# Optimization experiments

Measured on AMD Instinct MI355X. Metric: run time of the kernel, lower is better.

## Reference

```python
import jax, jax.numpy as jnp
import numpy as np

B, H, W, C = 16, 56, 56, 256
NH, WS, SS = 8, 7, 3          # heads, window size, shift size
HD = C // NH                  # head dim = 32
MLPD = 4 * C                  # mlp hidden = 1024
WA = WS * WS                  # window area = 49
NW = (H // WS) * (W // WS)    # windows per image = 64
SCALE = HD ** -0.5


def _rel_pos_index():
    coords = np.stack(np.meshgrid(np.arange(WS), np.arange(WS), indexing='ij'))
    cf = coords.reshape(2, -1)
    rel = (cf[:, :, None] - cf[:, None, :]).transpose(1, 2, 0)
    rel[:, :, 0] += WS - 1
    rel[:, :, 1] += WS - 1
    rel[:, :, 0] *= 2 * WS - 1
    return rel.sum(-1)  # (WA, WA) int


def _shift_attn_mask():
    img = np.zeros((H, W))
    cnt = 0
    for hs in (slice(0, -WS), slice(-WS, -SS), slice(-SS, None)):
        for ws_ in (slice(0, -WS), slice(-WS, -SS), slice(-SS, None)):
            img[hs, ws_] = cnt
            cnt += 1
    mw = img.reshape(H // WS, WS, W // WS, WS).transpose(0, 2, 1, 3).reshape(-1, WA)
    am = mw[:, None, :] - mw[:, :, None]
    return np.where(am != 0, -100.0, 0.0).astype(np.float32)  # (NW, WA, WA)

REL_IDX = jnp.asarray(_rel_pos_index())
ATTN_MASK = jnp.asarray(_shift_attn_mask())


def setup_inputs() -> dict:
    key = jax.random.key(0)
    ks = jax.random.split(key, 8)
    s = 0.02
    return {
        'x':      jax.random.normal(ks[0], (B, H * W, C), jnp.float32),
        'g1':     jnp.ones((C,), jnp.float32),
        'be1':    jnp.zeros((C,), jnp.float32),
        'w_qkv':  jax.random.normal(ks[1], (C, 3 * C), jnp.float32) * s,
        'b_qkv':  jnp.zeros((3 * C,), jnp.float32),
        'rpt':    jax.random.normal(ks[2], ((2 * WS - 1) ** 2, NH), jnp.float32) * s,
        'w_proj': jax.random.normal(ks[3], (C, C), jnp.float32) * s,
        'b_proj': jnp.zeros((C,), jnp.float32),
        'g2':     jnp.ones((C,), jnp.float32),
        'be2':    jnp.zeros((C,), jnp.float32),
        'w_fc1':  jax.random.normal(ks[4], (C, MLPD), jnp.float32) * s,
        'b_fc1':  jnp.zeros((MLPD,), jnp.float32),
        'w_fc2':  jax.random.normal(ks[5], (MLPD, C), jnp.float32) * s,
        'b_fc2':  jnp.zeros((C,), jnp.float32),
    }


def _ln(x, g, b, eps=1e-5):
    m = x.mean(-1, keepdims=True)
    v = ((x - m) ** 2).mean(-1, keepdims=True)
    return (x - m) * jax.lax.rsqrt(v + eps) * g + b


def reference(x, g1, be1, w_qkv, b_qkv, rpt, w_proj, b_proj, g2, be2,
              w_fc1, b_fc1, w_fc2, b_fc2):
    shortcut = x
    h = _ln(x, g1, be1).reshape(B, H, W, C)
    # cyclic shift
    h = jnp.roll(h, (-SS, -SS), axis=(1, 2))
    # window partition -> (B*NW, WA, C)
    h = h.reshape(B, H // WS, WS, W // WS, WS, C).transpose(0, 1, 3, 2, 4, 5)
    h = h.reshape(B * NW, WA, C)
    # qkv
    qkv = h @ w_qkv + b_qkv                       # (B*NW, WA, 3C)
    qkv = qkv.reshape(B * NW, WA, 3, NH, HD).transpose(2, 0, 3, 1, 4)
    q, k, v = qkv[0], qkv[1], qkv[2]              # (B*NW, NH, WA, HD)
    attn = jnp.einsum('wnqd,wnkd->wnqk', q * SCALE, k)   # (B*NW, NH, WA, WA)
    # relative position bias
    bias = rpt[REL_IDX.reshape(-1)].reshape(WA, WA, NH).transpose(2, 0, 1)
    attn = attn + bias[None]
    # shifted-window mask, per window
    attn = attn.reshape(B, NW, NH, WA, WA) + ATTN_MASK[None, :, None]
    attn = jax.nn.softmax(attn.reshape(B * NW, NH, WA, WA), axis=-1)
    out = jnp.einsum('wnqk,wnkd->wnqd', attn, v)  # (B*NW, NH, WA, HD)
    out = out.transpose(0, 2, 1, 3).reshape(B * NW, WA, C)
    out = out @ w_proj + b_proj
    # window reverse + unshift
    out = out.reshape(B, H // WS, W // WS, WS, WS, C).transpose(0, 1, 3, 2, 4, 5)
    out = out.reshape(B, H, W, C)
    out = jnp.roll(out, (SS, SS), axis=(1, 2)).reshape(B, H * W, C)
    x = shortcut + out
    # MLP block
    h2 = _ln(x, g2, be2)
    h2 = jax.nn.gelu(h2 @ w_fc1 + b_fc1, approximate=False) @ w_fc2 + b_fc2
    return x + h2
```

## Files before the change

### kernel.cpp

```cpp
#include <hip/hip_runtime.h>
#include <hip/hip_bf16.h>
#include <cstdint>
#include <cstddef>
#include <type_traits>

typedef __attribute__((ext_vector_type(8))) short short8;
typedef __attribute__((ext_vector_type(4))) float f32x4;
typedef __attribute__((ext_vector_type(4))) unsigned short us4;

#define DEVINL __device__ __forceinline__

static constexpr int SS_ = 3;
static constexpr int HH = 56, WW = 56;
#define SCALE_Q 0.17677669529663689f

DEVINL unsigned short f2b(float f) {
    unsigned int u = __builtin_bit_cast(unsigned int, f);
    unsigned int r = (u + 0x7FFFu + ((u >> 16) & 1u)) >> 16;
    return (unsigned short)r;
}
DEVINL float b2f(unsigned short s) {
    return __builtin_bit_cast(float, ((unsigned int)s) << 16);
}

DEVINL float gelu(float v) {
    float ax = fabsf(v) * 0.70710678118654752f;
    float t = 1.0f / (1.0f + 0.3275911f * ax);
    float poly = t * (0.254829592f +
                 t * (-0.284496736f +
                 t * (1.421413741f +
                 t * (-1.453152027f + t * 1.061405429f))));
    float e = __expf(-ax * ax);
    float erfv = 1.0f - poly * e;
    erfv = v >= 0.0f ? erfv : -erfv;
    return 0.5f * v * (1.0f + erfv);
}

DEVINL void gload_lds16(const unsigned short* g, unsigned short* l) {
    __builtin_amdgcn_global_load_lds(
        (const __attribute__((address_space(1))) unsigned int*)g,
        (__attribute__((address_space(3))) unsigned int*)l, 16, 0, 0);
}

__global__ void wconv_kernel(const float* __restrict__ in,
                             unsigned short* __restrict__ out, int K, int N) {
    int i = blockIdx.x * 256 + threadIdx.x;
    if (i >= K * N) return;
    int k = i / N, n = i - k * N;
    out[(size_t)n * K + k] = f2b(in[i]);
}

template <int MODE, typename TIN>
__global__ __launch_bounds__(256) void ln_kernel(
    const TIN* __restrict__ x, const float* __restrict__ g,
    const float* __restrict__ be, unsigned short* __restrict__ out) {
    const int wid = threadIdx.x >> 6, lane = threadIdx.x & 63;
    const int t = blockIdx.x * 4 + wid;
    int src;
    if constexpr (MODE == 1) {
        int w = t / 49, p = t - w * 49;
        int b = w >> 6, widx = w & 63;
        int wy = widx >> 3, wx = widx & 7;
        int py = p / 7, px = p - py * 7;
        int y = wy * 7 + py + SS_;  if (y >= HH) y -= HH;
        int xx = wx * 7 + px + SS_; if (xx >= WW) xx -= WW;
        src = b * (HH * WW) + y * WW + xx;
    } else {
        src = t;
    }
    float4 v;
    if constexpr (std::is_same_v<TIN, float>) {
        v = reinterpret_cast<const float4*>(x + (size_t)src * 256)[lane];
    } else {
        us4 u = reinterpret_cast<const us4*>(x + (size_t)src * 256)[lane];
        v.x = b2f(u.x); v.y = b2f(u.y); v.z = b2f(u.z); v.w = b2f(u.w);
    }
    float s = v.x + v.y + v.z + v.w;
    float q = v.x * v.x + v.y * v.y + v.z * v.z + v.w * v.w;
#pragma unroll
    for (int m = 1; m < 64; m <<= 1) {
        s += __shfl_xor(s, m);
        q += __shfl_xor(q, m);
    }
    float mean = s * (1.0f / 256.0f);
    float var = q * (1.0f / 256.0f) - mean * mean;
    float rs = rsqrtf(var + 1e-5f);
    int c = lane * 4;
    us4 o;
    o.x = f2b((v.x - mean) * rs * g[c + 0] + be[c + 0]);
    o.y = f2b((v.y - mean) * rs * g[c + 1] + be[c + 1]);
    o.z = f2b((v.z - mean) * rs * g[c + 2] + be[c + 2]);
    o.w = f2b((v.w - mean) * rs * g[c + 3] + be[c + 3]);
    *reinterpret_cast<us4*>(out + (size_t)t * 256 + c) = o;
}

template <int KDIM, int EPI>
__global__ __launch_bounds__(512) void gemm_kernel(
    const unsigned short* __restrict__ A, const unsigned short* __restrict__ Bt,
    const float* __restrict__ bias, void* __restrict__ out0,
    const void* __restrict__ res, unsigned short* __restrict__ o_q,
    unsigned short* __restrict__ o_k, unsigned short* __restrict__ o_v) {
    constexpr int BM = 256, BN = 128, BK = 32, NK = KDIM / BK;
    __shared__ __align__(16) unsigned short As[2][BM * BK];
    __shared__ __align__(16) unsigned short Bs[2][BN * BK];
    const int tid = threadIdx.x;
    const int wid = tid >> 6, lane = tid & 63;

    const int nwg = gridDim.x * gridDim.y;
    const int bid = blockIdx.x + gridDim.x * blockIdx.y;
    const int nb = (bid & 7) * (nwg >> 3) + (bid >> 3);
    const int n0 = (nb % gridDim.x) * BN;
    const int m0 = (nb / gridDim.x) * BM;

    const int wm = wid >> 1, wn = wid & 1;
    const int lr = lane & 15, kg = lane >> 4;
    f32x4 acc[4][4] = {};

    const int arow0 = tid >> 2, aslot = tid & 3;

    auto STAGE = [&](int kt, int buf) {
#pragma unroll
        for (int i = 0; i < 2; i++) {
            int row = i * 128 + arow0;
            int c = aslot ^ ((row >> 1) & 3);
            gload_lds16(A + (size_t)(m0 + row) * KDIM + kt * BK + c * 8,
                        As[buf] + i * 4096 + tid * 8);
        }
        {
            int row = arow0;
            int c = aslot ^ ((row >> 1) & 3);
            gload_lds16(Bt + (size_t)(n0 + row) * KDIM + kt * BK + c * 8,
                        Bs[buf] + tid * 8);
        }
    };

    STAGE(0, 0);
    __syncthreads();
    int cur = 0;
    for (int kt = 0; kt < NK; kt++) {
        if (kt + 1 < NK) STAGE(kt + 1, cur ^ 1);
        short8 a[4], b[4];
#pragma unroll
        for (int mf = 0; mf < 4; mf++) {
            int r = wm * 64 + mf * 16 + lr;
            a[mf] = *reinterpret_cast<const short8*>(
                As[cur] + r * 32 + ((kg ^ ((r >> 1) & 3)) << 3));
        }
#pragma unroll
        for (int nf = 0; nf < 4; nf++) {
            int r = wn * 64 + nf * 16 + lr;
            b[nf] = *reinterpret_cast<const short8*>(
                Bs[cur] + r * 32 + ((kg ^ ((r >> 1) & 3)) << 3));
        }
#pragma unroll
        for (int mf = 0; mf < 4; mf++)
#pragma unroll
            for (int nf = 0; nf < 4; nf++)
                acc[mf][nf] = __builtin_amdgcn_mfma_f32_16x16x32_bf16(
                    a[mf], b[nf], acc[mf][nf], 0, 0, 0);
        __syncthreads();
        cur ^= 1;
    }

#pragma unroll
    for (int mf = 0; mf < 4; mf++) {
#pragma unroll
        for (int nf = 0; nf < 4; nf++) {
#pragma unroll
            for (int j = 0; j < 4; j++) {
                int row = m0 + wm * 64 + mf * 16 + kg * 4 + j;
                int col = n0 + wn * 64 + nf * 16 + lr;
                float v = acc[mf][nf][j] + bias[col];
                if constexpr (EPI == 0) {
                    int w = row / 49, p = row - w * 49;
                    int which = col >> 8, h = (col >> 5) & 7, d = col & 31;
                    size_t th = (size_t)(w * 8 + h);
                    if (which == 0)
                        o_q[th * 1568 + p * 32 + d] = f2b(v * SCALE_Q);
                    else if (which == 1)
                        o_k[th * 1568 + p * 32 + d] = f2b(v);
                    else
                        o_v[th * 2048 + d * 64 + p] = f2b(v);
                } else if constexpr (EPI == 1) {
                    int w = row / 49, p = row - w * 49;
                    int b2 = w >> 6, widx = w & 63;
                    int wy = widx >> 3, wx = widx & 7;
                    int py = p / 7, px = p - py * 7;
                    int y = wy * 7 + py + SS_;  if (y >= HH) y -= HH;
                    int xx = wx * 7 + px + SS_; if (xx >= WW) xx -= WW;
                    size_t oi = ((size_t)(b2 * 3136 + y * 56 + xx)) * 256 + col;
                    reinterpret_cast<unsigned short*>(out0)[oi] =
                        f2b(v + reinterpret_cast<const float*>(res)[oi]);
                } else if constexpr (EPI == 2) {
                    reinterpret_cast<unsigned short*>(out0)[(size_t)row * 1024 + col] =
                        f2b(gelu(v));
                } else {
                    size_t oi = (size_t)row * 256 + col;
                    reinterpret_cast<float*>(out0)[oi] =
                        v + b2f(reinterpret_cast<const unsigned short*>(res)[oi]);
                }
            }
        }
    }
}

__global__ __launch_bounds__(256) void attn_kernel(
    const unsigned short* __restrict__ qg, const unsigned short* __restrict__ kgl,
    const unsigned short* __restrict__ vg, const float* __restrict__ rpt,
    unsigned short* __restrict__ out) {
    __shared__ __align__(16) unsigned short sm[4][6144];
    __shared__ unsigned short rpts[169 * 8];
    const int tid = threadIdx.x, wid = tid >> 6, lane = tid & 63;
    for (int i = tid; i < 169 * 8; i += 256) rpts[i] = f2b(rpt[i]);
    const int task = blockIdx.x * 4 + wid;
    const int w = task >> 3, h = task & 7;
    const int widx = w & 63, wy = widx >> 3, wx = widx & 7;
    unsigned short* q_s = sm[wid];
    unsigned short* k_s = sm[wid] + 2048;
    unsigned short* v_s = sm[wid] + 4096;
    unsigned short* p_s = sm[wid];
    const unsigned short* qsrc = qg + (size_t)task * 1568;
    const unsigned short* ksrc = kgl + (size_t)task * 1568;
    const unsigned short* vsrc = vg + (size_t)task * 2048;
    for (int c = lane; c < 196; c += 64) {
        int row = c >> 2, kc = c & 3;
        int off = (row * 32 + kc * 8) ^ ((row & 7) << 3);
        *reinterpret_cast<short8*>(q_s + off) =
            *reinterpret_cast<const short8*>(qsrc + c * 8);
        *reinterpret_cast<short8*>(k_s + off) =
            *reinterpret_cast<const short8*>(ksrc + c * 8);
    }
#pragma unroll
    for (int i = 0; i < 4; i++) {
        int c = i * 64 + lane;
        int row = c >> 3, kc = c & 7;
        int off = (row * 64 + kc * 8) ^ ((row & 7) << 3);
        *reinterpret_cast<short8*>(v_s + off) =
            *reinterpret_cast<const short8*>(vsrc + c * 8);
    }
    __syncthreads();

    const int lr = lane & 15, kg = lane >> 4;
    short8 af[4], bf[4];
#pragma unroll
    for (int mf = 0; mf < 4; mf++) {
        int r = mf * 16 + lr;
        af[mf] = *reinterpret_cast<const short8*>(
            q_s + ((r * 32 + kg * 8) ^ ((r & 7) << 3)));
    }
#pragma unroll
    for (int nf = 0; nf < 4; nf++) {
        int r = nf * 16 + lr;
        bf[nf] = *reinterpret_cast<const short8*>(
            k_s + ((r * 32 + kg * 8) ^ ((r & 7) << 3)));
    }
    f32x4 s[4][4] = {};
#pragma unroll
    for (int mf = 0; mf < 4; mf++)
#pragma unroll
        for (int nf = 0; nf < 4; nf++)
            s[mf][nf] = __builtin_amdgcn_mfma_f32_16x16x32_bf16(af[mf], bf[nf],
                                                                s[mf][nf], 0, 0, 0);
#pragma unroll
    for (int mf = 0; mf < 4; mf++) {
#pragma unroll
        for (int j = 0; j < 4; j++) {
            int row = mf * 16 + kg * 4 + j;
            bool rvalid = row < 49;
            int qy = 0, qx = 0, gq = 0;
            if (rvalid) {
                qy = row / 7; qx = row - qy * 7;
                int yi = wy * 7 + qy, xi = wx * 7 + qx;
                gq = ((yi < 49) ? 0 : ((yi < 53) ? 1 : 2)) * 3 +
                     ((xi < 49) ? 0 : ((xi < 53) ? 1 : 2));
            }
            float L[4];
#pragma unroll
            for (int nf = 0; nf < 4; nf++) {
                int col = nf * 16 + lr;
                float val = s[mf][nf][j];
                if (rvalid && col < 49) {
                    int ky = col / 7, kx = col - ky * 7;
                    int yi = wy * 7 + ky, xi = wx * 7 + kx;
                    int gk = ((yi < 49) ? 0 : ((yi < 53) ? 1 : 2)) * 3 +
                             ((xi < 49) ? 0 : ((xi < 53) ? 1 : 2));
                    val += b2f(rpts[((qy - ky + 6) * 13 + (qx - kx + 6)) * 8 + h]);
                    if (gq != gk) val -= 100.0f;
                } else {
                    val = -1e30f;
                }
                L[nf] = val;
            }
            float m = fmaxf(fmaxf(L[0], L[1]), fmaxf(L[2], L[3]));
#pragma unroll
            for (int t2 = 1; t2 < 16; t2 <<= 1) m = fmaxf(m, __shfl_xor(m, t2));
            float P[4], psum = 0.f;
#pragma unroll
            for (int nf = 0; nf < 4; nf++) {
                P[nf] = __expf(L[nf] - m);
                psum += P[nf];
            }
#pragma unroll
            for (int t2 = 1; t2 < 16; t2 <<= 1) psum += __shfl_xor(psum, t2);
            float inv = 1.0f / psum;
#pragma unroll
            for (int nf = 0; nf < 4; nf++) {
                int col = nf * 16 + lr;
                p_s[(row * 64 + col) ^ ((row & 7) << 3)] = f2b(P[nf] * inv);
            }
        }
    }
    f32x4 o[4][2] = {};
#pragma unroll
    for (int ks = 0; ks < 2; ks++) {
        short8 pa[4], vb[2];
#pragma unroll
        for (int mf = 0; mf < 4; mf++) {
            int r = mf * 16 + lr;
            pa[mf] = *reinterpret_cast<const short8*>(
                p_s + ((r * 64 + ks * 32 + kg * 8) ^ ((r & 7) << 3)));
        }
#pragma unroll
        for (int nf = 0; nf < 2; nf++) {
            int d = nf * 16 + lr;
            vb[nf] = *reinterpret_cast<const short8*>(
                v_s + ((d * 64 + ks * 32 + kg * 8) ^ ((d & 7) << 3)));
        }
#pragma unroll
        for (int mf = 0; mf < 4; mf++)
#pragma unroll
            for (int nf = 0; nf < 2; nf++)
                o[mf][nf] = __builtin_amdgcn_mfma_f32_16x16x32_bf16(
                    pa[mf], vb[nf], o[mf][nf], 0, 0, 0);
    }
#pragma unroll
    for (int mf = 0; mf < 4; mf++) {
#pragma unroll
        for (int j = 0; j < 4; j++) {
            int row = mf * 16 + kg * 4 + j;
            if (row < 49) {
#pragma unroll
                for (int nf = 0; nf < 2; nf++) {
                    int d = nf * 16 + lr;
                    out[((size_t)w * 49 + row) * 256 + h * 32 + d] =
                        f2b(o[mf][nf][j]);
                }
            }
        }
    }
}

extern "C" void kernel_launch(void* const* d_in, const int* in_sizes, int n_in,
                              void* d_out, int out_size, void* d_ws,
                              size_t ws_size, hipStream_t stream) {
    const float* x     = (const float*)d_in[0];
    const float* g1    = (const float*)d_in[1];
    const float* be1   = (const float*)d_in[2];
    const float* wqkv  = (const float*)d_in[3];
    const float* bqkv  = (const float*)d_in[4];
    const float* rpt   = (const float*)d_in[5];
    const float* wproj = (const float*)d_in[6];
    const float* bproj = (const float*)d_in[7];
    const float* g2    = (const float*)d_in[8];
    const float* be2   = (const float*)d_in[9];
    const float* wfc1  = (const float*)d_in[10];
    const float* bfc1  = (const float*)d_in[11];
    const float* wfc2  = (const float*)d_in[12];
    const float* bfc2  = (const float*)d_in[13];
    float* out = (float*)d_out;
    char* ws = (char*)d_ws;

    unsigned short* hb  = (unsigned short*)(ws);
    unsigned short* qg  = (unsigned short*)(ws + 25690112);
    unsigned short* kgl = (unsigned short*)(ws + 51380224);
    unsigned short* vg  = (unsigned short*)(ws + 77070336);
    unsigned short* x2b = (unsigned short*)(ws + 110624768);
    unsigned short* h2  = (unsigned short*)(ws + 162004992);
    unsigned short* wT  = (unsigned short*)(ws + 187695104);
    unsigned short* wqkvT = wT;
    unsigned short* wprojT = wT + 196608;
    unsigned short* wfc1T  = wT + 262144;
    unsigned short* wfc2T  = wT + 524288;
    unsigned short* a1 = (unsigned short*)ws;

    wconv_kernel<<<(256 * 768 + 255) / 256, 256, 0, stream>>>(wqkv, wqkvT, 256, 768);
    wconv_kernel<<<(256 * 256 + 255) / 256, 256, 0, stream>>>(wproj, wprojT, 256, 256);
    wconv_kernel<<<(256 * 1024 + 255) / 256, 256, 0, stream>>>(wfc1, wfc1T, 256, 1024);
    wconv_kernel<<<(1024 * 256 + 255) / 256, 256, 0, stream>>>(wfc2, wfc2T, 1024, 256);

    ln_kernel<1, float><<<12544, 256, 0, stream>>>(x, g1, be1, hb);
    gemm_kernel<256, 0><<<dim3(6, 196), 512, 0, stream>>>(
        hb, wqkvT, bqkv, nullptr, nullptr, qg, kgl, vg);
    attn_kernel<<<2048, 256, 0, stream>>>(qg, kgl, vg, rpt, hb);
    gemm_kernel<256, 1><<<dim3(2, 196), 512, 0, stream>>>(
        hb, wprojT, bproj, x2b, x, nullptr, nullptr, nullptr);
    ln_kernel<0, unsigned short><<<12544, 256, 0, stream>>>(x2b, g2, be2, h2);
    gemm_kernel<256, 2><<<dim3(8, 196), 512, 0, stream>>>(
        h2, wfc1T, bfc1, a1, nullptr, nullptr, nullptr, nullptr);
    gemm_kernel<1024, 3><<<dim3(2, 196), 512, 0, stream>>>(
        a1, wfc2T, bfc2, out, x2b, nullptr, nullptr, nullptr);
}
```

Before: 321.1 us.

## Retile GEMM to 128x128x64 single-buffered blocks and use cheaper erf approximation

The GEMM kernel moves from 256x128 tiles with BK=32 double buffering and 512 threads to 128x128 tiles with BK=64, a single LDS buffer, 256 threads and launch bounds allowing 4 blocks per CU. The LDS swizzle changes to match the wider K tile, and the grids double along M. Separately, the GELU erf approximation is swapped from the 5-term Abramowitz-Stegun polynomial to a lower-accuracy 3-term one. The retiling trades in-block prefetch overlap for more resident blocks per CU, and the erf change lowers accuracy.

```diff
diff --git a/kernel.cpp b/kernel.cpp
--- a/kernel.cpp
+++ b/kernel.cpp
@@ -25,13 +25,9 @@
 
 DEVINL float gelu(float v) {
     float ax = fabsf(v) * 0.70710678118654752f;
-    float t = 1.0f / (1.0f + 0.3275911f * ax);
-    float poly = t * (0.254829592f +
-                 t * (-0.284496736f +
-                 t * (1.421413741f +
-                 t * (-1.453152027f + t * 1.061405429f))));
-    float e = __expf(-ax * ax);
-    float erfv = 1.0f - poly * e;
+    float t = 1.0f / (1.0f + 0.47047f * ax);
+    float poly = t * (0.3480242f + t * (-0.0958798f + t * 0.7478556f));
+    float erfv = 1.0f - poly * __expf(-ax * ax);
     erfv = v >= 0.0f ? erfv : -erfv;
     return 0.5f * v * (1.0f + erfv);
 }
@@ -95,14 +91,14 @@
 }
 
 template <int KDIM, int EPI>
-__global__ __launch_bounds__(512) void gemm_kernel(
+__global__ __launch_bounds__(256, 4) void gemm_kernel(
     const unsigned short* __restrict__ A, const unsigned short* __restrict__ Bt,
     const float* __restrict__ bias, void* __restrict__ out0,
     const void* __restrict__ res, unsigned short* __restrict__ o_q,
     unsigned short* __restrict__ o_k, unsigned short* __restrict__ o_v) {
-    constexpr int BM = 256, BN = 128, BK = 32, NK = KDIM / BK;
-    __shared__ __align__(16) unsigned short As[2][BM * BK];
-    __shared__ __align__(16) unsigned short Bs[2][BN * BK];
+    constexpr int BM = 128, BN = 128, BK = 64;
+    __shared__ __align__(16) unsigned short As[BM * BK];
+    __shared__ __align__(16) unsigned short Bs[BN * BK];
     const int tid = threadIdx.x;
     const int wid = tid >> 6, lane = tid & 63;
 
@@ -116,50 +112,46 @@
     const int lr = lane & 15, kg = lane >> 4;
     f32x4 acc[4][4] = {};
 
-    const int arow0 = tid >> 2, aslot = tid & 3;
-
-    auto STAGE = [&](int kt, int buf) {
-#pragma unroll
-        for (int i = 0; i < 2; i++) {
-            int row = i * 128 + arow0;
-            int c = aslot ^ ((row >> 1) & 3);
-            gload_lds16(A + (size_t)(m0 + row) * KDIM + kt * BK + c * 8,
-                        As[buf] + i * 4096 + tid * 8);
-        }
-        {
-            int row = arow0;
-            int c = aslot ^ ((row >> 1) & 3);
-            gload_lds16(Bt + (size_t)(n0 + row) * KDIM + kt * BK + c * 8,
-                        Bs[buf] + tid * 8);
-        }
-    };
-
-    STAGE(0, 0);
-    __syncthreads();
-    int cur = 0;
-    for (int kt = 0; kt < NK; kt++) {
-        if (kt + 1 < NK) STAGE(kt + 1, cur ^ 1);
-        short8 a[4], b[4];
-#pragma unroll
-        for (int mf = 0; mf < 4; mf++) {
-            int r = wm * 64 + mf * 16 + lr;
-            a[mf] = *reinterpret_cast<const short8*>(
-                As[cur] + r * 32 + ((kg ^ ((r >> 1) & 3)) << 3));
-        }
-#pragma unroll
-        for (int nf = 0; nf < 4; nf++) {
-            int r = wn * 64 + nf * 16 + lr;
-            b[nf] = *reinterpret_cast<const short8*>(
-                Bs[cur] + r * 32 + ((kg ^ ((r >> 1) & 3)) << 3));
-        }
-#pragma unroll
-        for (int mf = 0; mf < 4; mf++)
-#pragma unroll
-            for (int nf = 0; nf < 4; nf++)
-                acc[mf][nf] = __builtin_amdgcn_mfma_f32_16x16x32_bf16(
-                    a[mf], b[nf], acc[mf][nf], 0, 0, 0);
+    const int srow = tid >> 3;
+    const int spos = tid & 7;
+
+    for (int kt = 0; kt < KDIM; kt += BK) {
+#pragma unroll
+        for (int i = 0; i < 4; i++) {
+            int row = i * 32 + srow;
+            gload_lds16(A + (size_t)(m0 + row) * KDIM + kt + ((spos ^ (row & 7)) << 3),
+                        As + i * 2048 + tid * 8);
+        }
+#pragma unroll
+        for (int i = 0; i < 4; i++) {
+            int row = i * 32 + srow;
+            gload_lds16(Bt + (size_t)(n0 + row) * KDIM + kt + ((spos ^ (row & 7)) << 3),
+                        Bs + i * 2048 + tid * 8);
+        }
         __syncthreads();
-        cur ^= 1;
+#pragma unroll
+        for (int ks = 0; ks < 2; ks++) {
+            short8 a[4], b[4];
+#pragma unroll
+            for (int mf = 0; mf < 4; mf++) {
+                int r = wm * 64 + mf * 16 + lr;
+                a[mf] = *reinterpret_cast<const short8*>(
+                    As + r * 64 + (((ks * 4 + kg) ^ (r & 7)) << 3));
+            }
+#pragma unroll
+            for (int nf = 0; nf < 4; nf++) {
+                int r = wn * 64 + nf * 16 + lr;
+                b[nf] = *reinterpret_cast<const short8*>(
+                    Bs + r * 64 + (((ks * 4 + kg) ^ (r & 7)) << 3));
+            }
+#pragma unroll
+            for (int mf = 0; mf < 4; mf++)
+#pragma unroll
+                for (int nf = 0; nf < 4; nf++)
+                    acc[mf][nf] = __builtin_amdgcn_mfma_f32_16x16x32_bf16(
+                        a[mf], b[nf], acc[mf][nf], 0, 0, 0);
+        }
+        __syncthreads();
     }
 
 #pragma unroll
@@ -389,14 +381,14 @@
     wconv_kernel<<<(1024 * 256 + 255) / 256, 256, 0, stream>>>(wfc2, wfc2T, 1024, 256);
 
     ln_kernel<1, float><<<12544, 256, 0, stream>>>(x, g1, be1, hb);
-    gemm_kernel<256, 0><<<dim3(6, 196), 512, 0, stream>>>(
+    gemm_kernel<256, 0><<<dim3(6, 392), 256, 0, stream>>>(
         hb, wqkvT, bqkv, nullptr, nullptr, qg, kgl, vg);
     attn_kernel<<<2048, 256, 0, stream>>>(qg, kgl, vg, rpt, hb);
-    gemm_kernel<256, 1><<<dim3(2, 196), 512, 0, stream>>>(
+    gemm_kernel<256, 1><<<dim3(2, 392), 256, 0, stream>>>(
         hb, wprojT, bproj, x2b, x, nullptr, nullptr, nullptr);
     ln_kernel<0, unsigned short><<<12544, 256, 0, stream>>>(x2b, g2, be2, h2);
-    gemm_kernel<256, 2><<<dim3(8, 196), 512, 0, stream>>>(
+    gemm_kernel<256, 2><<<dim3(8, 392), 256, 0, stream>>>(
         h2, wfc1T, bfc1, a1, nullptr, nullptr, nullptr, nullptr);
-    gemm_kernel<1024, 3><<<dim3(2, 196), 512, 0, stream>>>(
+    gemm_kernel<1024, 3><<<dim3(2, 392), 256, 0, stream>>>(
         a1, wfc2T, bfc2, out, x2b, nullptr, nullptr, nullptr);
 }
```

Result: faster. 288.0 us (-10.3%).
